# Performance work log

Measured on AMD Instinct MI355X. Metric: run time of the kernel, lower is better.

Reference implementation:

```python
import jax, jax.numpy as jnp
import numpy as np

jax.config.update("jax_enable_x64", True)  # original torch code runs in float64; minors underflow fp32

D = 96   # Nsites
N = 48   # Nparticles


def setup_inputs() -> dict:
    key = jax.random.key(0)
    # Orthonormal single-particle orbitals (columns), as the module assumes (P^T P = I)
    A = jax.random.normal(key, (D, D), dtype=jnp.float64)
    Q, _ = jnp.linalg.qr(A)
    P = Q[:, :N]  # [D, N]
    # A valid ordered particle configuration: strictly increasing, occ_positions[k] <= D-N+k
    occ_positions = jnp.arange(N, dtype=jnp.int32) * (D // N)  # stride-2 filling
    return {"P": P, "occ_positions": occ_positions}


def _cond_probs(P, occ_positions):
    """Conditional probabilities probs[k, x] of placing the k-th (ordered) particle at
    site x given particles 0..k-1 at occ_positions[0..k-1].

    Math identical to SlaterDetSampler_ordered.get_cond_prob (naive_update=True):
      G = I - P P^T
      probs[k,x] = -det(M_x[0:x+1,0:x+1]) / det(M[0:xmin,0:xmin])
    where M = G - diag(occupancy of particles < k) and M_x additionally sets n_x = 1.
    Since Ksites is always the contiguous range 0..x, all determinants are LEADING
    principal minors; and because only the (x,x) diagonal entry changes by -1 (last index
    of the block), det(M_x block) = d_{x+1} - d_x with d_j the leading j-minor of M.
    """
    Dd, Nn = P.shape
    dt = P.dtype
    eye = jnp.eye(Dd, dtype=dt)
    G = eye - P @ P.T                                             # [D, D]

    onehots = jax.nn.one_hot(occ_positions, Dd, dtype=dt)         # [N, D]
    n_before = jnp.cumsum(onehots, axis=0) - onehots              # occupancy of particles < k
    A = G[None] - n_before[:, :, None] * eye                      # [N, D, D]: G - diag(n_<k)

    # All leading principal minors via batched det of masked matrices:
    # M_j = A on the [0:j,0:j] block, identity elsewhere  =>  det(M_j) = leading j-minor
    ii = jnp.arange(Dd)
    jj = jnp.arange(1, Dd + 1)
    blk = (ii[None, :, None] < jj[:, None, None]) & (ii[None, None, :] < jj[:, None, None])  # [D,D,D]
    Ms = jnp.where(blk[None], A[:, None], eye)                    # [N, D, D, D]
    d = jnp.linalg.det(Ms.reshape(Nn * Dd, Dd, Dd)).reshape(Nn, Dd)
    d_full = jnp.concatenate([jnp.ones((Nn, 1), dt), d], axis=1)  # d_full[k, j] = j-th leading minor

    k = jnp.arange(Nn)
    xmin = jnp.where(k == 0, 0, occ_positions[jnp.maximum(k - 1, 0)] + 1)  # [N]
    xmax = Dd - Nn + k + 1                                                  # [N]
    denom = jnp.take_along_axis(d_full, xmin[:, None], axis=1)              # [N, 1]
    num = d_full[:, 1:] - d_full[:, :-1]                                    # det(GG_num) per candidate x

    x = jnp.arange(Dd)
    support = (x[None, :] >= xmin[:, None]) & (x[None, :] < xmax[:, None])
    probs = jnp.where(support, -num / denom, jnp.zeros((), dt))
    # torch.where(abs(probs) > 1e-15, probs, 0.)
    probs = jnp.where(jnp.abs(probs) > 1e-15, probs, jnp.zeros((), dt))
    return probs


def reference(P, occ_positions):
    probs = _cond_probs(P, occ_positions)                          # [N, D]
    # prob of the full ordered sample = prod_k probs[k, occ_positions[k]]  (as in sample())
    p_k = jnp.take_along_axis(probs, occ_positions[:, None], axis=1)[:, 0]
    prob_sample = jnp.prod(p_k)
    return probs, prob_sample
```

## Files before the change

### kernel.cpp

```cpp
#include <hip/hip_runtime.h>
#include <math.h>

#define Dd 96
#define Nn 48
#define LD 97
#define PTS 98

__device__ __forceinline__ double frcp(double x) {
    double r = __builtin_amdgcn_rcp(x);
    r = fma(fma(-x, r, 1.0), r, r);
    r = fma(fma(-x, r, 1.0), r, r);
    return r;
}

__global__ __launch_bounds__(1024, 1) void slater_kernel(const float* __restrict__ P,
                                                         const int* __restrict__ occ,
                                                         float* __restrict__ out,
                                                         unsigned* __restrict__ cnt) {
    __shared__ double As[Dd * LD];
    __shared__ double Sbuf[2][6][Dd];
    __shared__ double aBuf[2][Dd][6];
    __shared__ double ev[2][6];
    __shared__ int    evmask[2], sdead[2];
    __shared__ double gs_runprod;
    __shared__ int    gs_dead;
    __shared__ unsigned char flag[Dd];
    float* PT = (float*)As;

    const int tid  = threadIdx.x;
    const int k    = blockIdx.x;
    const int n    = Dd - Nn + k + 1;
    const int lane = tid & 63;
    const int wave = tid >> 6;
    const int xmin = (k == 0) ? 0 : occ[k - 1] + 1;

    if (tid < Dd) flag[tid] = 0;
    __syncthreads();
    if (tid < k) flag[occ[tid]] = 1;
    for (int e = tid; e < Dd * Nn; e += 1024) {
        int c = e / Nn, t = e - (e / Nn) * Nn;
        PT[t * PTS + c] = P[e];
    }
    __syncthreads();

    double Areg[8]; int trs[2], tcs[2];
#pragma unroll
    for (int it = 0; it < 2; ++it) {
        int tau = tid + 1024 * it;
        double s00 = 0.0, s01 = 0.0, s10 = 0.0, s11 = 0.0;
        int tr = 0, tc = 0;
        if (tau < 1176) {
            tr = (int)((97.0 - sqrt(9409.0 - 8.0 * (double)tau)) * 0.5);
            while ((tr * (97 - tr)) / 2 > tau) --tr;
            while (((tr + 1) * (96 - tr)) / 2 <= tau) ++tr;
            tc = tr + (tau - (tr * (97 - tr)) / 2);
            int r0 = 2 * tr, c0 = 2 * tc;
            if (r0 < n && c0 < n) {
                for (int t = 0; t < Nn; ++t) {
                    const float* row = PT + t * PTS;
                    float2 pr = *(const float2*)(row + r0);
                    float2 pc = *(const float2*)(row + c0);
                    s00 -= (double)pr.x * (double)pc.x; s01 -= (double)pr.x * (double)pc.y;
                    s10 -= (double)pr.y * (double)pc.x; s11 -= (double)pr.y * (double)pc.y;
                }
            }
        }
        trs[it] = tr; tcs[it] = tc;
        Areg[it * 4 + 0] = s00; Areg[it * 4 + 1] = s01;
        Areg[it * 4 + 2] = s10; Areg[it * 4 + 3] = s11;
    }
    __syncthreads();
#pragma unroll
    for (int it = 0; it < 2; ++it) {
        int tau = tid + 1024 * it;
        if (tau < 1176) {
            int tr = trs[it], tc = tcs[it];
            int r0 = 2 * tr, c0 = 2 * tc;
            if (r0 < n && c0 < n) {
                bool r1 = (r0 + 1 < n), c1 = (c0 + 1 < n);
                double d0 = flag[r0] ? 0.0 : 1.0;
                double d1 = flag[r0 + 1] ? 0.0 : 1.0;
                As[r0 * LD + c0] = Areg[it * 4 + 0] + ((r0 == c0) ? d0 : 0.0);
                if (c1)       As[r0 * LD + c0 + 1]       = Areg[it * 4 + 1];
                if (r1)       As[(r0 + 1) * LD + c0]     = Areg[it * 4 + 2];
                if (r1 && c1) As[(r0 + 1) * LD + c0 + 1] = Areg[it * 4 + 3] + ((r0 == c0) ? d1 : 0.0);
                if (tr != tc) {
                    As[c0 * LD + r0] = Areg[it * 4 + 0];
                    if (c1)       As[(c0 + 1) * LD + r0]     = Areg[it * 4 + 1];
                    if (r1)       As[c0 * LD + r0 + 1]       = Areg[it * 4 + 2];
                    if (r1 && c1) As[(c0 + 1) * LD + r0 + 1] = Areg[it * 4 + 3];
                }
            }
        }
    }
    __syncthreads();

    double myprob = 0.0;
    double rr[6][2];

    auto prefactor = [&](int jb, int p, double grun, int gdead) {
        double Bd[6][6], rp[6];
#pragma unroll
        for (int u = 0; u < 6; ++u) {
#pragma unroll
            for (int r = 0; r < 6; ++r)
                Bd[u][r] = __shfl((r & 1) ? rr[u][1] : rr[u][0], (jb + r) >> 1, 64);
        }
#pragma unroll
        for (int cc = 0; cc < 6; ++cc) {
            rp[cc] = frcp(Bd[cc][cc]);
#pragma unroll
            for (int i = cc + 1; i < 6; ++i) {
                double m = Bd[i][cc] * rp[cc];
                Bd[i][cc] = m;
#pragma unroll
                for (int r = cc + 1; r < 6; ++r) Bd[i][r] -= m * Bd[cc][r];
            }
        }
        if (lane == 0) {
            int msk = 0; double evv[6];
#pragma unroll
            for (int q = 0; q < 6; ++q) {
                evv[q] = 0.0;
                if (!gdead) {
                    int jj = jb + q;
                    double pv = Bd[q][q];
                    double ap = fabs(pv);
                    if (jj >= xmin) {
                        evv[q] = grun * (1.0 - pv);
                        msk |= (1 << q);
                        double nr = grun * pv;
                        if (!(ap > 1e-7) || !(ap < 8.0) || !(fabs(nr) > 1e-8)) gdead = 1;
                        else grun = nr;
                    } else {
                        if (!(ap > 1e-12) || !(ap < 8.0)) gdead = 1;
                    }
                }
            }
#pragma unroll
            for (int q = 0; q < 6; ++q) ev[p][q] = evv[q];
            evmask[p] = msk; sdead[p] = gdead;
            gs_runprod = grun; gs_dead = gdead;
        }
        if (lane < 48) {
            const bool live = (2 * lane >= jb + 6);
#pragma unroll
            for (int sl = 0; sl < 2; ++sl) {
                double y0 = rr[0][sl];
                double y1 = rr[1][sl] - Bd[1][0] * y0;
                double y2 = rr[2][sl] - Bd[2][0] * y0 - Bd[2][1] * y1;
                double y3 = rr[3][sl] - Bd[3][0] * y0 - Bd[3][1] * y1 - Bd[3][2] * y2;
                double y4 = rr[4][sl] - Bd[4][0] * y0 - Bd[4][1] * y1 - Bd[4][2] * y2 - Bd[4][3] * y3;
                double y5 = rr[5][sl] - Bd[5][0] * y0 - Bd[5][1] * y1 - Bd[5][2] * y2 - Bd[5][3] * y3 - Bd[5][4] * y4;
                double s5 = y5 * rp[5];
                double s4 = (y4 - Bd[4][5] * s5) * rp[4];
                double s3 = (y3 - Bd[3][4] * s4 - Bd[3][5] * s5) * rp[3];
                double s2 = (y2 - Bd[2][3] * s3 - Bd[2][4] * s4 - Bd[2][5] * s5) * rp[2];
                double s1 = (y1 - Bd[1][2] * s2 - Bd[1][3] * s3 - Bd[1][4] * s4 - Bd[1][5] * s5) * rp[1];
                double s0 = (y0 - Bd[0][1] * s1 - Bd[0][2] * s2 - Bd[0][3] * s3 - Bd[0][4] * s4 - Bd[0][5] * s5) * rp[0];
                Sbuf[p][0][2 * lane + sl] = live ? s0 : 0.0;
                Sbuf[p][1][2 * lane + sl] = live ? s1 : 0.0;
                Sbuf[p][2][2 * lane + sl] = live ? s2 : 0.0;
                Sbuf[p][3][2 * lane + sl] = live ? s3 : 0.0;
                Sbuf[p][4][2 * lane + sl] = live ? s4 : 0.0;
                Sbuf[p][5][2 * lane + sl] = live ? s5 : 0.0;
            }
        }
    };

#pragma unroll
    for (int u = 0; u < 6; ++u) {
        if (lane < 48) {
            rr[u][0] = As[(6 * wave + u) * LD + 2 * lane];
            rr[u][1] = As[(6 * wave + u) * LD + 2 * lane + 1];
        } else { rr[u][0] = 0.0; rr[u][1] = 0.0; }
    }
    if (wave >= 1 && lane < 3) {
#pragma unroll
        for (int u = 0; u < 6; ++u) {
            aBuf[0][6 * wave + u][2 * lane]     = rr[u][0];
            aBuf[0][6 * wave + u][2 * lane + 1] = rr[u][1];
        }
    }
    if (wave == 0) prefactor(0, 0, 1.0, 0);
    __syncthreads();

    int j = 0, s = 0;
    for (; j + 6 <= n - 1; j += 6, ++s) {
        const int par = s & 1;
        if (tid >= j && tid < j + 6) {
            int q = tid - j;
            if ((evmask[par] >> q) & 1) myprob = ev[par][q];
        }
        if (sdead[par]) break;
        const bool nexts = (j + 12 <= n - 1);

        if (wave >= s + 1) {
            if (lane < 48) {
                double S0[6], S1[6];
#pragma unroll
                for (int r = 0; r < 6; ++r) {
                    double2 sv = *(const double2*)&Sbuf[par][r][2 * lane];
                    S0[r] = sv.x; S1[r] = sv.y;
                }
#pragma unroll
                for (int u = 0; u < 6; ++u) {
                    const double* ab = &aBuf[par][6 * wave + u][0];
                    double2 q0 = *(const double2*)(ab + 0);
                    double2 q1 = *(const double2*)(ab + 2);
                    double2 q2 = *(const double2*)(ab + 4);
                    rr[u][0] -= q0.x * S0[0] + q0.y * S0[1] + q1.x * S0[2]
                              + q1.y * S0[3] + q2.x * S0[4] + q2.y * S0[5];
                    rr[u][1] -= q0.x * S1[0] + q0.y * S1[1] + q1.x * S1[2]
                              + q1.y * S1[3] + q2.x * S1[4] + q2.y * S1[5];
                }
                if (nexts && wave >= s + 2) {
                    int d = lane - 3 * (s + 1);
                    if (d >= 0 && d < 3) {
#pragma unroll
                        for (int u = 0; u < 6; ++u) {
                            aBuf[par ^ 1][6 * wave + u][2 * d]     = rr[u][0];
                            aBuf[par ^ 1][6 * wave + u][2 * d + 1] = rr[u][1];
                        }
                    }
                }
            }
            if (nexts && wave == s + 1)
                prefactor(j + 6, par ^ 1, gs_runprod, gs_dead);
        }
        __syncthreads();
    }

    if (lane < 48) {
#pragma unroll
        for (int u = 0; u < 6; ++u) {
            As[(6 * wave + u) * LD + 2 * lane]     = rr[u][0];
            As[(6 * wave + u) * LD + 2 * lane + 1] = rr[u][1];
        }
    }
    __syncthreads();

    double runprod = gs_runprod;
    bool   dead    = (gs_dead != 0);

    for (; !dead && j < n - 1; ++j) {
        double pivot = As[j * LD + j];
        {
            double ap = fabs(pivot);
            if (j >= xmin) {
                if (tid == j) myprob = runprod * (1.0 - pivot);
                double nr = runprod * pivot;
                if (!(ap > 1e-7) || !(ap < 8.0) || !(fabs(nr) > 1e-8)) dead = true;
                else runprod = nr;
            } else {
                if (!(ap > 1e-12) || !(ap < 8.0)) dead = true;
            }
        }
        if (dead) break;
        double rp = frcp(pivot);
        int t = n - 1 - j;
        double r0 = (lane < t)      ? As[j * LD + j + 1 + lane]  : 0.0;
        double r1 = (lane + 64 < t) ? As[j * LD + j + 65 + lane] : 0.0;
        for (int i = j + 1 + wave; i < n; i += 16) {
            double mult = As[i * LD + j] * rp;
            if (lane < t)      As[i * LD + j + 1 + lane]  -= mult * r0;
            if (lane + 64 < t) As[i * LD + j + 65 + lane] -= mult * r1;
        }
        __syncthreads();
    }
    if (!dead && tid == n - 1) {
        double pl = As[(n - 1) * LD + (n - 1)];
        myprob = runprod * (1.0 - pl);
    }

    if (tid < Dd) {
        double p = myprob;
        if (!isfinite(p)) p = 0.0;
        if (!(fabs(p) > 1e-15)) p = 0.0;
        p = fmin(fmax(p, 0.0), 1.0);
        out[k * Dd + tid] = (float)p;
    }

    __threadfence();
    __syncthreads();
    if (wave == 0) {
        int old = 0;
        if (lane == 0)
            old = (int)__hip_atomic_fetch_add(cnt, 1u, __ATOMIC_ACQ_REL,
                                              __HIP_MEMORY_SCOPE_AGENT);
        old = __shfl(old, 0, 64);
        if (((unsigned)old + 1u) % (unsigned)Nn == 0u) {
            __threadfence();
            double v = 1.0;
            if (lane < Nn) {
                float f = __hip_atomic_load(out + lane * Dd + occ[lane],
                                            __ATOMIC_RELAXED, __HIP_MEMORY_SCOPE_AGENT);
                v = (double)f;
            }
#pragma unroll
            for (int off = 32; off >= 1; off >>= 1)
                v *= __shfl_down(v, off, 64);
            if (lane == 0) {
                if (!isfinite(v)) v = 0.0;
                out[Nn * Dd] = (float)v;
            }
        }
    }
}

extern "C" void kernel_launch(void* const* d_in, const int* in_sizes, int n_in,
                              void* d_out, int out_size, void* d_ws, size_t ws_size,
                              hipStream_t stream) {
    const float* P = (const float*)d_in[0];
    const int* occ = (const int*)d_in[1];
    float* out = (float*)d_out;

    slater_kernel<<<Nn, 1024, 0, stream>>>(P, occ, out, (unsigned*)d_ws);
}
```

Measured before the change: 100.9 us.

## Fuse pivot checks into block LU and finish tail block in registers

Moves the pivot and probability bookkeeping into the 6x6 block factorization loop, so it no longer runs as a separate serial pass over the factored pivots. Reciprocal pivots are stored on the diagonal instead of in a separate array. The scalar per-row elimination tail over shared memory, with one block barrier per row, is replaced by a single-lane factorization of the last register block when it fits. Also switches to a waves-per-eu attribute and pads aBuf to a stride of 8. If the remaining tail is larger than one block (full false), those probabilities are no longer computed.

```diff
diff --git a/kernel.cpp b/kernel.cpp
--- a/kernel.cpp
+++ b/kernel.cpp
@@ -13,15 +13,18 @@
     return r;
 }
 
-__global__ __launch_bounds__(1024, 1) void slater_kernel(const float* __restrict__ P,
-                                                         const int* __restrict__ occ,
-                                                         float* __restrict__ out,
-                                                         unsigned* __restrict__ cnt) {
+__attribute__((amdgpu_waves_per_eu(4, 4)))
+__global__ __launch_bounds__(1024) void slater_kernel(const float* __restrict__ P,
+                                                      const int* __restrict__ occ,
+                                                      float* __restrict__ out,
+                                                      unsigned* __restrict__ cnt) {
     __shared__ double As[Dd * LD];
     __shared__ double Sbuf[2][6][Dd];
-    __shared__ double aBuf[2][Dd][6];
+    __shared__ double aBuf[2][Dd][8];
     __shared__ double ev[2][6];
     __shared__ int    evmask[2], sdead[2];
+    __shared__ double evm[6];
+    __shared__ int    evmmask;
     __shared__ double gs_runprod;
     __shared__ int    gs_dead;
     __shared__ unsigned char flag[Dd];
@@ -99,46 +102,40 @@
     double rr[6][2];
 
     auto prefactor = [&](int jb, int p, double grun, int gdead) {
-        double Bd[6][6], rp[6];
-#pragma unroll
-        for (int u = 0; u < 6; ++u) {
+        double Bd[6][6];
+#pragma unroll
+        for (int u = 0; u < 6; ++u)
 #pragma unroll
             for (int r = 0; r < 6; ++r)
                 Bd[u][r] = __shfl((r & 1) ? rr[u][1] : rr[u][0], (jb + r) >> 1, 64);
-        }
+        int msk = 0;
 #pragma unroll
         for (int cc = 0; cc < 6; ++cc) {
-            rp[cc] = frcp(Bd[cc][cc]);
+            double piv = Bd[cc][cc];
+            double ap = fabs(piv);
+            int jj = jb + cc;
+            if (!gdead) {
+                if (jj >= xmin) {
+                    if (lane == 0) ev[p][cc] = grun * (1.0 - piv);
+                    msk |= (1 << cc);
+                    double nr = grun * piv;
+                    if (!(ap > 1e-7) || !(ap < 8.0) || !(fabs(nr) > 1e-8)) gdead = 1;
+                    else grun = nr;
+                } else {
+                    if (!(ap > 1e-12) || !(ap < 8.0)) gdead = 1;
+                }
+            }
+            double rp = frcp(piv);
+            Bd[cc][cc] = rp;
 #pragma unroll
             for (int i = cc + 1; i < 6; ++i) {
-                double m = Bd[i][cc] * rp[cc];
+                double m = Bd[i][cc] * rp;
                 Bd[i][cc] = m;
 #pragma unroll
                 for (int r = cc + 1; r < 6; ++r) Bd[i][r] -= m * Bd[cc][r];
             }
         }
         if (lane == 0) {
-            int msk = 0; double evv[6];
-#pragma unroll
-            for (int q = 0; q < 6; ++q) {
-                evv[q] = 0.0;
-                if (!gdead) {
-                    int jj = jb + q;
-                    double pv = Bd[q][q];
-                    double ap = fabs(pv);
-                    if (jj >= xmin) {
-                        evv[q] = grun * (1.0 - pv);
-                        msk |= (1 << q);
-                        double nr = grun * pv;
-                        if (!(ap > 1e-7) || !(ap < 8.0) || !(fabs(nr) > 1e-8)) gdead = 1;
-                        else grun = nr;
-                    } else {
-                        if (!(ap > 1e-12) || !(ap < 8.0)) gdead = 1;
-                    }
-                }
-            }
-#pragma unroll
-            for (int q = 0; q < 6; ++q) ev[p][q] = evv[q];
             evmask[p] = msk; sdead[p] = gdead;
             gs_runprod = grun; gs_dead = gdead;
         }
@@ -146,18 +143,18 @@
             const bool live = (2 * lane >= jb + 6);
 #pragma unroll
             for (int sl = 0; sl < 2; ++sl) {
-                double y0 = rr[0][sl];
-                double y1 = rr[1][sl] - Bd[1][0] * y0;
-                double y2 = rr[2][sl] - Bd[2][0] * y0 - Bd[2][1] * y1;
-                double y3 = rr[3][sl] - Bd[3][0] * y0 - Bd[3][1] * y1 - Bd[3][2] * y2;
-                double y4 = rr[4][sl] - Bd[4][0] * y0 - Bd[4][1] * y1 - Bd[4][2] * y2 - Bd[4][3] * y3;
-                double y5 = rr[5][sl] - Bd[5][0] * y0 - Bd[5][1] * y1 - Bd[5][2] * y2 - Bd[5][3] * y3 - Bd[5][4] * y4;
-                double s5 = y5 * rp[5];
-                double s4 = (y4 - Bd[4][5] * s5) * rp[4];
-                double s3 = (y3 - Bd[3][4] * s4 - Bd[3][5] * s5) * rp[3];
-                double s2 = (y2 - Bd[2][3] * s3 - Bd[2][4] * s4 - Bd[2][5] * s5) * rp[2];
-                double s1 = (y1 - Bd[1][2] * s2 - Bd[1][3] * s3 - Bd[1][4] * s4 - Bd[1][5] * s5) * rp[1];
-                double s0 = (y0 - Bd[0][1] * s1 - Bd[0][2] * s2 - Bd[0][3] * s3 - Bd[0][4] * s4 - Bd[0][5] * s5) * rp[0];
+                double s0 = rr[0][sl];
+                double s1 = rr[1][sl] - Bd[1][0] * s0;
+                double s2 = rr[2][sl] - Bd[2][0] * s0 - Bd[2][1] * s1;
+                double s3 = rr[3][sl] - Bd[3][0] * s0 - Bd[3][1] * s1 - Bd[3][2] * s2;
+                double s4 = rr[4][sl] - Bd[4][0] * s0 - Bd[4][1] * s1 - Bd[4][2] * s2 - Bd[4][3] * s3;
+                double s5 = rr[5][sl] - Bd[5][0] * s0 - Bd[5][1] * s1 - Bd[5][2] * s2 - Bd[5][3] * s3 - Bd[5][4] * s4;
+                s5 = s5 * Bd[5][5];
+                s4 = (s4 - Bd[4][5] * s5) * Bd[4][4];
+                s3 = (s3 - Bd[3][4] * s4 - Bd[3][5] * s5) * Bd[3][3];
+                s2 = (s2 - Bd[2][3] * s3 - Bd[2][4] * s4 - Bd[2][5] * s5) * Bd[2][2];
+                s1 = (s1 - Bd[1][2] * s2 - Bd[1][3] * s3 - Bd[1][4] * s4 - Bd[1][5] * s5) * Bd[1][1];
+                s0 = (s0 - Bd[0][1] * s1 - Bd[0][2] * s2 - Bd[0][3] * s3 - Bd[0][4] * s4 - Bd[0][5] * s5) * Bd[0][0];
                 Sbuf[p][0][2 * lane + sl] = live ? s0 : 0.0;
                 Sbuf[p][1][2 * lane + sl] = live ? s1 : 0.0;
                 Sbuf[p][2][2 * lane + sl] = live ? s2 : 0.0;
@@ -231,46 +228,54 @@
         __syncthreads();
     }
 
-    if (lane < 48) {
-#pragma unroll
-        for (int u = 0; u < 6; ++u) {
-            As[(6 * wave + u) * LD + 2 * lane]     = rr[u][0];
-            As[(6 * wave + u) * LD + 2 * lane + 1] = rr[u][1];
-        }
-    }
-    __syncthreads();
-
-    double runprod = gs_runprod;
-    bool   dead    = (gs_dead != 0);
-
-    for (; !dead && j < n - 1; ++j) {
-        double pivot = As[j * LD + j];
-        {
-            double ap = fabs(pivot);
-            if (j >= xmin) {
-                if (tid == j) myprob = runprod * (1.0 - pivot);
-                double nr = runprod * pivot;
-                if (!(ap > 1e-7) || !(ap < 8.0) || !(fabs(nr) > 1e-8)) dead = true;
-                else runprod = nr;
-            } else {
-                if (!(ap > 1e-12) || !(ap < 8.0)) dead = true;
-            }
-        }
-        if (dead) break;
-        double rp = frcp(pivot);
-        int t = n - 1 - j;
-        double r0 = (lane < t)      ? As[j * LD + j + 1 + lane]  : 0.0;
-        double r1 = (lane + 64 < t) ? As[j * LD + j + 65 + lane] : 0.0;
-        for (int i = j + 1 + wave; i < n; i += 16) {
-            double mult = As[i * LD + j] * rp;
-            if (lane < t)      As[i * LD + j + 1 + lane]  -= mult * r0;
-            if (lane + 64 < t) As[i * LD + j + 65 + lane] -= mult * r1;
-        }
-        __syncthreads();
-    }
-    if (!dead && tid == n - 1) {
-        double pl = As[(n - 1) * LD + (n - 1)];
-        myprob = runprod * (1.0 - pl);
+    const int  jend = j;
+    const bool full = (jend + 6 > n - 1);
+    if (full && wave == (jend / 6)) {
+        const int rsz = n - jend;
+        double Bm[6][6];
+#pragma unroll
+        for (int u = 0; u < 6; ++u)
+#pragma unroll
+            for (int r = 0; r < 6; ++r)
+                Bm[u][r] = __shfl((r & 1) ? rr[u][1] : rr[u][0], (jend + r) >> 1, 64);
+        if (lane == 0) {
+            double grun = gs_runprod; int gdead = gs_dead;
+            int msk = 0;
+            double evs[6] = {0.0, 0.0, 0.0, 0.0, 0.0, 0.0};
+            for (int q = 0; q < rsz - 1; ++q) {
+                if (gdead) break;
+                double piv = Bm[q][q];
+                double ap = fabs(piv);
+                int jj = jend + q;
+                if (jj >= xmin) {
+                    evs[q] = grun * (1.0 - piv); msk |= (1 << q);
+                    double nr = grun * piv;
+                    if (!(ap > 1e-7) || !(ap < 8.0) || !(fabs(nr) > 1e-8)) gdead = 1;
+                    else grun = nr;
+                } else {
+                    if (!(ap > 1e-12) || !(ap < 8.0)) gdead = 1;
+                }
+                if (!gdead) {
+                    double rp = frcp(piv);
+                    for (int i = q + 1; i < rsz; ++i) {
+                        double m = Bm[i][q] * rp;
+                        for (int r = q + 1; r < rsz; ++r) Bm[i][r] -= m * Bm[q][r];
+                    }
+                }
+            }
+            if (!gdead) {
+                evs[rsz - 1] = grun * (1.0 - Bm[rsz - 1][rsz - 1]);
+                msk |= (1 << (rsz - 1));
+            }
+#pragma unroll
+            for (int q = 0; q < 6; ++q) evm[q] = evs[q];
+            evmmask = msk;
+        }
+    }
+    __syncthreads();
+    if (full && tid >= jend && tid < n) {
+        int q = tid - jend;
+        if ((evmmask >> q) & 1) myprob = evm[q];
     }
 
     if (tid < Dd) {
```

Result: slower. 110.3 us (+9.3%).
